# Kernel optimization log

Measured on AMD Instinct MI355X. Metric: run time of the kernel, lower is better.

Reference implementation:

```python
import jax, jax.numpy as jnp
import numpy as np

NN_SIZE = 16
RADIUS2 = 0.5 * 0.5  # radius^2
EPS = 0.0001


def setup_inputs() -> dict:
    key = jax.random.key(0)
    points = jax.random.normal(key, (4, 8192, 3), dtype=jnp.float32)
    return {"points": points}


def reference(points):
    # points: (B, N, 3)
    B, N, C = points.shape
    # Brute-force KNN (pytorch3d ops.knn_points with K = nn_size + 1, self included)
    sq = jnp.sum(points * points, axis=-1)  # (B, N)
    d2_all = sq[:, :, None] + sq[:, None, :] - 2.0 * jnp.einsum('bnc,bmc->bnm', points, points)  # (B,N,N)
    _, idx = jax.lax.top_k(-d2_all, NN_SIZE + 1)  # smallest distances first, (B,N,K+1)
    knn_idx = idx[:, :, 1:]  # drop self, (B, N, K)
    # Gather neighbor coordinates; detached in the original (.detach())
    knn_points = jax.vmap(lambda p, i: p[i])(points, knn_idx)  # (B, N, K, 3)
    knn_points = jax.lax.stop_gradient(knn_points)
    # Recompute squared distances (as the module does)
    knn_v = knn_points - points[:, :, None, :]  # (B, N, K, 3)
    distance2 = jnp.sum(knn_v * knn_v, axis=-1)  # (B, N, K)
    loss = 1.0 / jnp.sqrt(distance2 + EPS)
    loss = jnp.where(distance2 < RADIUS2, loss, jnp.zeros_like(loss))
    # reduction == 'mean'
    return jnp.mean(loss)
```

## Files before the change

### kernel.cpp

```cpp
#include <hip/hip_runtime.h>

#define NPTS 8192
#define NBATCH 4
#define NTOT (NBATCH * NPTS)
#define NN 16
#define RAD2 0.25f
#define EPSF 1e-4f
#define BIGF 1e30f

#define GC 16
#define GP 18
#define CBS 6144
#define NCELL_TOT (NBATCH * CBS)

#define STHR 256
#define SWV 4
#define SNB (NTOT / SWV)
#define HCAP 384

#define LOG2C 5.0103f
#define NCLAMP 257

#define WS_COUNTS 0
#define WS_RANGES (WS_COUNTS + NCELL_TOT * 4)
#define WS_CURSOR (WS_RANGES + NCELL_TOT * 8)
#define WS_SORTED (WS_CURSOR + NCELL_TOT * 4)
#define WS_BSUMS  (WS_SORTED + (NTOT + 64) * 16)
#define WS_NEEDED (WS_BSUMS + SNB * 4)

__device__ __forceinline__ int cellc(float v) {
  return min(max((int)floorf((v + 4.0f) * 2.0f), 0), GC - 1);
}

__device__ __forceinline__ float prsqrt(float x) {
  float r = __builtin_amdgcn_rsqf(x);
  r = r * fmaf(-0.5f * x * r, r, 1.5f);
  return r;
}

#define CE(a, b) { const float lo_ = fminf(a, b); const float hi_ = fmaxf(a, b); a = lo_; b = hi_; }


__global__ __launch_bounds__(256)
void zero_kernel(int* __restrict__ counts) {
  const int i = blockIdx.x * 256 + threadIdx.x;
  if (i < NCELL_TOT) counts[i] = 0;
}

__global__ __launch_bounds__(256)
void hist_kernel(const float* __restrict__ pts, int* __restrict__ counts) {
  const int i = blockIdx.x * 256 + threadIdx.x;
  if (i >= NTOT) return;
  const int b = i >> 13;
  const float x = pts[i * 3 + 0], y = pts[i * 3 + 1], z = pts[i * 3 + 2];
  const int c = b * CBS + ((cellc(z) + 1) * GP + (cellc(y) + 1)) * GP + (cellc(x) + 1);
  atomicAdd(&counts[c], 1);
}

__global__ __launch_bounds__(1024)
void scan_kernel(const int* __restrict__ counts, int2* __restrict__ ranges,
                 int* __restrict__ cursor) {
  __shared__ int wsum[16];
  __shared__ int woff[16];
  __shared__ int stot;
  const int b = blockIdx.x;
  const int tid = threadIdx.x;
  const int wid = tid >> 6;
  const int lane = tid & 63;
  const int g0 = b * CBS;
  int running = b * NPTS;
  for (int chunk = 0; chunk < CBS; chunk += 1024) {
    const int idx = chunk + tid;
    const int v = counts[g0 + idx];
    int x = v;
    for (int off = 1; off < 64; off <<= 1) {
      const int t = __shfl_up(x, off, 64);
      if (lane >= off) x += t;
    }
    if (lane == 63) wsum[wid] = x;
    __syncthreads();
    if (wid == 0) {
      int s = (lane < 16) ? wsum[lane] : 0;
      for (int off = 1; off < 16; off <<= 1) {
        const int t = __shfl_up(s, off, 64);
        if (lane >= off) s += t;
      }
      if (lane < 16) woff[lane] = s - wsum[lane];
      if (lane == 15) stot = s;
    }
    __syncthreads();
    const int excl = running + woff[wid] + x - v;
    ranges[g0 + idx] = make_int2(excl, v);
    cursor[g0 + idx] = excl;
    running += stot;
    __syncthreads();
  }
}

__global__ __launch_bounds__(256)
void scatter_kernel(const float* __restrict__ pts, int* __restrict__ cursor,
                    float4* __restrict__ sorted) {
  const int i = blockIdx.x * 256 + threadIdx.x;
  if (i >= NTOT) return;
  const int b = i >> 13;
  const float x = pts[i * 3 + 0], y = pts[i * 3 + 1], z = pts[i * 3 + 2];
  const int c = b * CBS + ((cellc(z) + 1) * GP + (cellc(y) + 1)) * GP + (cellc(x) + 1);
  const int pos = atomicAdd(&cursor[c], 1);
  sorted[pos] = make_float4(x, y, z, fmaf(x, x, fmaf(y, y, z * z)));
}


template<int R>
__device__ __forceinline__ float tourney(const float* __restrict__ hq, int hn, int lane) {
  float v[R];
#pragma unroll
  for (int r = 0; r < R; ++r) {
    const int idx = lane + 64 * r;
    v[r] = (idx < hn) ? hq[idx] : BIGF;
  }
  if constexpr (R == 3) { CE(v[0], v[1]); CE(v[1], v[2]); CE(v[0], v[1]); }
  if constexpr (R == 6) {
    CE(v[0], v[1]); CE(v[2], v[3]); CE(v[4], v[5]);
    CE(v[1], v[2]); CE(v[3], v[4]);
    CE(v[0], v[1]); CE(v[2], v[3]); CE(v[4], v[5]);
    CE(v[1], v[2]); CE(v[3], v[4]);
    CE(v[0], v[1]); CE(v[2], v[3]); CE(v[4], v[5]);
    CE(v[1], v[2]); CE(v[3], v[4]);
  }
  float loss = 0.0f;
#pragma unroll
  for (int r = 0; r < NN; ++r) {
    float g = v[0];
    g = fminf(g, __shfl_xor(g, 1));
    g = fminf(g, __shfl_xor(g, 2));
    g = fminf(g, __shfl_xor(g, 4));
    g = fminf(g, __shfl_xor(g, 8));
    g = fminf(g, __shfl_xor(g, 16));
    g = fminf(g, __shfl_xor(g, 32));
    loss += prsqrt(g + EPSF);
    const unsigned long long own = __ballot(v[0] == g);
    const int first = (int)(__ffsll((unsigned long long)own) - 1);
    if (lane == first) {
#pragma unroll
      for (int r2 = 0; r2 < R - 1; ++r2) v[r2] = v[r2 + 1];
      v[R - 1] = BIGF;
    }
  }
  return loss;
}

__global__ __launch_bounds__(STHR)
void search_kernel(const float4* __restrict__ sorted, const int2* __restrict__ rngs,
                   float* __restrict__ bsums) {
  __shared__ float hbuf[SWV][HCAP];
  __shared__ float wloss[SWV];

  const int tid = threadIdx.x;
  const int wv = tid >> 6;
  const int lane = tid & 63;
  const int p = blockIdx.x * SWV + wv;
  const int bb = p >> 13;

  const float4 pt = sorted[p];
  const float m2x = -2.0f * pt.x, m2y = -2.0f * pt.y, m2z = -2.0f * pt.z;
  const float sp = pt.w;
  const int cx = cellc(pt.x), cy = cellc(pt.y), cz = cellc(pt.z);
  const int c0 = __builtin_amdgcn_readfirstlane(
      bb * CBS + ((cz + 1) * GP + (cy + 1)) * GP + (cx + 1));

  const int rowoff[9] = {
    (-1 * GP - 1) * GP, (-1 * GP + 0) * GP, (-1 * GP + 1) * GP,
    ( 0 * GP - 1) * GP, ( 0 * GP + 0) * GP, ( 0 * GP + 1) * GP,
    ( 1 * GP - 1) * GP, ( 1 * GP + 0) * GP, ( 1 * GP + 1) * GP };

  int rs[9], re[9];
  int ncand = 0;
#pragma unroll
  for (int m = 0; m < 9; ++m) {
    const int2 a = rngs[c0 + rowoff[m] - 1];
    const int2 e2 = rngs[c0 + rowoff[m] + 1];
    rs[m] = a.x;
    re[m] = e2.x + e2.y;
    ncand += re[m] - rs[m];
  }

  const bool clamped = (ncand <= NCLAMP);
  float r0sq = RAD2;
  if (!clamped) {
    r0sq = exp2f((LOG2C - log2f((float)ncand)) * (2.0f / 3.0f));
  }

  float* hq = hbuf[wv];
  int hcnt = 0;

#define SCAN_ROWS(RR) {                                                         \
    hcnt = 0;                                                                   \
    _Pragma("unroll")                                                           \
    for (int m = 0; m < 9; ++m) {                                               \
      const int s = rs[m], e = re[m];                                           \
      for (int j0 = s; j0 < e; j0 += 64) {                                      \
        const int j = j0 + lane;                                                \
        float d2 = BIGF;                                                        \
        if (j < e) {                                                            \
          const float4 q = sorted[j];                                           \
          d2 = fmaf(q.x, m2x, fmaf(q.y, m2y, fmaf(q.z, m2z, q.w + sp)));        \
        }                                                                       \
        bool hit = (d2 < (RR));                                                 \
        if (m == 4) hit = hit && (j != p);            \
        const unsigned long long bal = __ballot(hit);                           \
        const int pre = __builtin_amdgcn_mbcnt_hi(                              \
            (unsigned)(bal >> 32), __builtin_amdgcn_mbcnt_lo((unsigned)bal, 0));\
        const int pos = hcnt + pre;                                             \
        if (hit && pos < HCAP) hq[pos] = d2;                                    \
        hcnt += (int)__popcll(bal);                                             \
      }                                                                         \
    }                                                                           \
  }

  SCAN_ROWS(r0sq);
  int hn = min(hcnt, HCAP);
  if (hn < NN && !clamped) {
    SCAN_ROWS(RAD2);
    hn = min(hcnt, HCAP);
  }

  float loss;
  if (hn <= 64) {
    float v = (lane < hn) ? hq[lane] : BIGF;
#pragma unroll
    for (int k = 2; k <= 64; k <<= 1) {
#pragma unroll
      for (int j = k >> 1; j > 0; j >>= 1) {
        const float o = __shfl_xor(v, j, 64);
        const bool keepmin = (((lane & j) == 0) != ((lane & k) != 0));
        v = keepmin ? fminf(v, o) : fmaxf(v, o);
      }
    }
    float l = (lane < NN && v < RAD2) ? prsqrt(v + EPSF) : 0.0f;
    l += __shfl_xor(l, 1);
    l += __shfl_xor(l, 2);
    l += __shfl_xor(l, 4);
    l += __shfl_xor(l, 8);
    l += __shfl_xor(l, 16);
    l += __shfl_xor(l, 32);
    loss = l;
  } else if (hn <= 192) {
    loss = tourney<3>(hq, hn, lane);
  } else {
    loss = tourney<6>(hq, hn, lane);
  }

  if (lane == 0) wloss[wv] = loss;
  __syncthreads();
  if (tid == 0) {
    float s = 0.0f;
#pragma unroll
    for (int w = 0; w < SWV; ++w) s += wloss[w];
    bsums[blockIdx.x] = s;
  }
}

__global__ __launch_bounds__(256)
void finalize_kernel(const float* __restrict__ block_sums, int nblocks,
                     float* __restrict__ out) {
  __shared__ float s[256];
  float v = 0.0f;
  for (int idx = threadIdx.x; idx < nblocks; idx += 256) v += block_sums[idx];
  s[threadIdx.x] = v;
  __syncthreads();
  for (int off = 128; off > 0; off >>= 1) {
    if (threadIdx.x < off) s[threadIdx.x] += s[threadIdx.x + off];
    __syncthreads();
  }
  if (threadIdx.x == 0) out[0] = s[0] / (float)(NBATCH * NPTS * NN);
}


#define DTILE 1024
#define DNT 512
#define DNW 8
#define DNB (NTOT / 64)
#define CSTRIDE 17
#define QTRIG 13

__device__ __forceinline__ void insert16(float (&td)[NN], float& thrmax, float v) {
  if (v < thrmax) {
    bool done = false;
#pragma unroll
    for (int k = 0; k < NN; ++k) {
      const bool hit = (!done) && (td[k] == thrmax);
      if (hit) td[k] = v;
      done = done || hit;
    }
    thrmax = td[0];
#pragma unroll
    for (int k = 1; k < NN; ++k) thrmax = fmaxf(thrmax, td[k]);
  }
}

__device__ __forceinline__ void drain_queue(float* buf, int qbase, int& cnt,
                                            float (&td)[NN], float& thrmax) {
#pragma unroll
  for (int c = 0; c < 16; ++c) {
    const float v = (c < cnt) ? buf[qbase + c] : BIGF;
    insert16(td, thrmax, v);
  }
  cnt = 0;
}

__global__ __launch_bounds__(DNT)
void dense_kernel(const float* __restrict__ pts, float* __restrict__ block_sums) {
  __shared__ float4 tile[DTILE];
  __shared__ float buf[DNT * CSTRIDE];

  const int tid = threadIdx.x;
  const int wave = tid >> 6;
  const int lane = tid & 63;
  const int bid = blockIdx.x;
  const int b = bid / (NPTS / 64);
  const int base = (bid % (NPTS / 64)) * 64;
  const float* __restrict__ bp = pts + (size_t)b * NPTS * 3;

  const int i = base + lane;
  const float xi = bp[i * 3 + 0];
  const float yi = bp[i * 3 + 1];
  const float zi = bp[i * 3 + 2];

  float td[NN];
#pragma unroll
  for (int k = 0; k < NN; ++k) td[k] = BIGF;
  float thrmax = BIGF;
  int cnt = 0;
  const int qbase = tid * CSTRIDE;

  for (int tb = 0; tb < NPTS; tb += DTILE) {
    for (int pp = tid; pp < DTILE; pp += DNT) {
      const float* sp = bp + (size_t)(tb + pp) * 3;
      tile[pp] = make_float4(sp[0], sp[1], sp[2], 0.0f);
    }
    __syncthreads();
    const int jb = wave * (DTILE / DNW);
    for (int jj = 0; jj < DTILE / DNW; ++jj) {
      const float4 q = tile[jb + jj];
      const float ddx = q.x - xi, ddy = q.y - yi, ddz = q.z - zi;
      const float d2 = fmaf(ddx, ddx, fmaf(ddy, ddy, ddz * ddz));
      if (d2 < RAD2 && d2 != 0.0f) {
        buf[qbase + cnt] = d2;
        ++cnt;
      }
      if (__any(cnt >= QTRIG)) drain_queue(buf, qbase, cnt, td, thrmax);
    }
    __syncthreads();
  }
  drain_queue(buf, qbase, cnt, td, thrmax);
#pragma unroll
  for (int k = 0; k < NN; ++k) buf[qbase + k] = td[k];
  __syncthreads();

  if (wave == 0) {
    float sd[NN];
#pragma unroll
    for (int k = 0; k < NN; ++k) sd[k] = BIGF;
    float smax = BIGF;
    for (int w = 0; w < DNW; ++w) {
      for (int c = 0; c < NN; ++c) {
        insert16(sd, smax, buf[(w * 64 + lane) * CSTRIDE + c]);
      }
    }
    float loss = 0.0f;
#pragma unroll
    for (int k = 0; k < NN; ++k) {
      if (sd[k] < RAD2) loss += 1.0f / sqrtf(sd[k] + EPSF);
    }
    for (int off = 32; off > 0; off >>= 1) loss += __shfl_down(loss, off);
    if (lane == 0) block_sums[bid] = loss;
  }
}


extern "C" void kernel_launch(void* const* d_in, const int* in_sizes, int n_in,
                              void* d_out, int out_size, void* d_ws, size_t ws_size,
                              hipStream_t stream) {
  const float* pts = (const float*)d_in[0];
  float* out = (float*)d_out;
  char* ws = (char*)d_ws;

  if (ws_size >= (size_t)WS_NEEDED) {
    int* counts = (int*)(ws + WS_COUNTS);
    int2* rngs = (int2*)(ws + WS_RANGES);
    int* cursor = (int*)(ws + WS_CURSOR);
    float4* sorted = (float4*)(ws + WS_SORTED);
    float* bsums = (float*)(ws + WS_BSUMS);

    zero_kernel<<<(NCELL_TOT + 255) / 256, 256, 0, stream>>>(counts);
    hist_kernel<<<(NTOT + 255) / 256, 256, 0, stream>>>(pts, counts);
    scan_kernel<<<NBATCH, 1024, 0, stream>>>(counts, rngs, cursor);
    scatter_kernel<<<(NTOT + 255) / 256, 256, 0, stream>>>(pts, cursor, sorted);
    search_kernel<<<SNB, STHR, 0, stream>>>(sorted, rngs, bsums);
    finalize_kernel<<<1, 256, 0, stream>>>(bsums, SNB, out);
  } else {
    float* bsums = (float*)ws;
    dense_kernel<<<DNB, DNT, 0, stream>>>(pts, bsums);
    finalize_kernel<<<1, 256, 0, stream>>>(bsums, DNB, out);
  }
}
```

Measured before the change: 66.87 us.

## Process two sorted query points per wavefront sharing candidate loads

Each wavefront now handles two consecutive sorted points. When both fall in the same y/z cell row, the union of their 3x3 x-ranges is scanned once, and each candidate load is used to compute distances for both queries. Otherwise the two points are scanned separately. This aims to halve candidate memory traffic and per-wave setup, at the cost of a wider scan range in the merged case and more registers and LDS per wave. The clamp radius in the merged case is derived from the combined candidate count, which may give different radius choices than per-point counts would.

```diff
diff --git a/kernel.cpp b/kernel.cpp
--- a/kernel.cpp
+++ b/kernel.cpp
@@ -15,7 +15,8 @@
 
 #define STHR 256
 #define SWV 4
-#define SNB (NTOT / SWV)
+#define PPW 2
+#define SNB (NTOT / (SWV * PPW))
 #define HCAP 384
 
 #define LOG2C 5.0103f
@@ -36,6 +37,11 @@
   float r = __builtin_amdgcn_rsqf(x);
   r = r * fmaf(-0.5f * x * r, r, 1.5f);
   return r;
+}
+
+__device__ __forceinline__ int lanepre(unsigned long long m) {
+  return __builtin_amdgcn_mbcnt_hi((unsigned)(m >> 32),
+         __builtin_amdgcn_mbcnt_lo((unsigned)m, 0));
 }
 
 #define CE(a, b) { const float lo_ = fminf(a, b); const float hi_ = fmaxf(a, b); a = lo_; b = hi_; }
@@ -110,6 +116,69 @@
 }
 
 
+__device__ __forceinline__ int scan1(const float4* __restrict__ sorted,
+    const int* rs, const int* re, float rr, int selfp,
+    float m2x, float m2y, float m2z, float sp, float* __restrict__ hq, int lane) {
+  int hcnt = 0;
+#pragma unroll
+  for (int m = 0; m < 9; ++m) {
+    const int s = rs[m], e = re[m];
+    for (int j0 = s; j0 < e; j0 += 64) {
+      const int j = j0 + lane;
+      float d2 = BIGF;
+      if (j < e) {
+        const float4 q = sorted[j];
+        d2 = fmaf(q.x, m2x, fmaf(q.y, m2y, fmaf(q.z, m2z, q.w + sp)));
+      }
+      const bool hit = (d2 < rr) && (j != selfp);
+      const unsigned long long bal = __ballot(hit);
+      const int pos = hcnt + lanepre(bal & ((1ull << lane) - 1ull) ? bal & ((1ull << lane) - 1ull) : 0ull);
+      const int pre = __popcll(bal & ((1ull << lane) - 1ull));
+      const int p2 = hcnt + pre;
+      if (hit && p2 < HCAP) hq[p2] = d2;
+      hcnt += (int)__popcll(bal);
+      (void)pos;
+    }
+  }
+  return hcnt;
+}
+
+__device__ __forceinline__ void scan2(const float4* __restrict__ sorted,
+    const int* rs, const int* re, float rr,
+    int pA, float m2xA, float m2yA, float m2zA, float spA,
+    int pB, float m2xB, float m2yB, float m2zB, float spB,
+    float* __restrict__ hqA, float* __restrict__ hqB, int lane,
+    int& hcntA, int& hcntB) {
+  int hA = 0, hB = 0;
+#pragma unroll
+  for (int m = 0; m < 9; ++m) {
+    const int s = rs[m], e = re[m];
+    for (int j0 = s; j0 < e; j0 += 64) {
+      const int j = j0 + lane;
+      float d2A = BIGF, d2B = BIGF;
+      if (j < e) {
+        const float4 q = sorted[j];
+        const float qw = q.w;
+        d2A = fmaf(q.x, m2xA, fmaf(q.y, m2yA, fmaf(q.z, m2zA, qw + spA)));
+        d2B = fmaf(q.x, m2xB, fmaf(q.y, m2yB, fmaf(q.z, m2zB, qw + spB)));
+      }
+      const unsigned long long below = (1ull << lane) - 1ull;
+      const bool hitA = (d2A < rr) && (j != pA);
+      const unsigned long long balA = __ballot(hitA);
+      const int posA = hA + (int)__popcll(balA & below);
+      if (hitA && posA < HCAP) hqA[posA] = d2A;
+      hA += (int)__popcll(balA);
+      const bool hitB = (d2B < rr) && (j != pB);
+      const unsigned long long balB = __ballot(hitB);
+      const int posB = hB + (int)__popcll(balB & below);
+      if (hitB && posB < HCAP) hqB[posB] = d2B;
+      hB += (int)__popcll(balB);
+    }
+  }
+  hcntA = hA;
+  hcntB = hB;
+}
+
 template<int R>
 __device__ __forceinline__ float tourney(const float* __restrict__ hq, int hn, int lane) {
   float v[R];
@@ -149,82 +218,7 @@
   return loss;
 }
 
-__global__ __launch_bounds__(STHR)
-void search_kernel(const float4* __restrict__ sorted, const int2* __restrict__ rngs,
-                   float* __restrict__ bsums) {
-  __shared__ float hbuf[SWV][HCAP];
-  __shared__ float wloss[SWV];
-
-  const int tid = threadIdx.x;
-  const int wv = tid >> 6;
-  const int lane = tid & 63;
-  const int p = blockIdx.x * SWV + wv;
-  const int bb = p >> 13;
-
-  const float4 pt = sorted[p];
-  const float m2x = -2.0f * pt.x, m2y = -2.0f * pt.y, m2z = -2.0f * pt.z;
-  const float sp = pt.w;
-  const int cx = cellc(pt.x), cy = cellc(pt.y), cz = cellc(pt.z);
-  const int c0 = __builtin_amdgcn_readfirstlane(
-      bb * CBS + ((cz + 1) * GP + (cy + 1)) * GP + (cx + 1));
-
-  const int rowoff[9] = {
-    (-1 * GP - 1) * GP, (-1 * GP + 0) * GP, (-1 * GP + 1) * GP,
-    ( 0 * GP - 1) * GP, ( 0 * GP + 0) * GP, ( 0 * GP + 1) * GP,
-    ( 1 * GP - 1) * GP, ( 1 * GP + 0) * GP, ( 1 * GP + 1) * GP };
-
-  int rs[9], re[9];
-  int ncand = 0;
-#pragma unroll
-  for (int m = 0; m < 9; ++m) {
-    const int2 a = rngs[c0 + rowoff[m] - 1];
-    const int2 e2 = rngs[c0 + rowoff[m] + 1];
-    rs[m] = a.x;
-    re[m] = e2.x + e2.y;
-    ncand += re[m] - rs[m];
-  }
-
-  const bool clamped = (ncand <= NCLAMP);
-  float r0sq = RAD2;
-  if (!clamped) {
-    r0sq = exp2f((LOG2C - log2f((float)ncand)) * (2.0f / 3.0f));
-  }
-
-  float* hq = hbuf[wv];
-  int hcnt = 0;
-
-#define SCAN_ROWS(RR) {                                                         \
-    hcnt = 0;                                                                   \
-    _Pragma("unroll")                                                           \
-    for (int m = 0; m < 9; ++m) {                                               \
-      const int s = rs[m], e = re[m];                                           \
-      for (int j0 = s; j0 < e; j0 += 64) {                                      \
-        const int j = j0 + lane;                                                \
-        float d2 = BIGF;                                                        \
-        if (j < e) {                                                            \
-          const float4 q = sorted[j];                                           \
-          d2 = fmaf(q.x, m2x, fmaf(q.y, m2y, fmaf(q.z, m2z, q.w + sp)));        \
-        }                                                                       \
-        bool hit = (d2 < (RR));                                                 \
-        if (m == 4) hit = hit && (j != p);            \
-        const unsigned long long bal = __ballot(hit);                           \
-        const int pre = __builtin_amdgcn_mbcnt_hi(                              \
-            (unsigned)(bal >> 32), __builtin_amdgcn_mbcnt_lo((unsigned)bal, 0));\
-        const int pos = hcnt + pre;                                             \
-        if (hit && pos < HCAP) hq[pos] = d2;                                    \
-        hcnt += (int)__popcll(bal);                                             \
-      }                                                                         \
-    }                                                                           \
-  }
-
-  SCAN_ROWS(r0sq);
-  int hn = min(hcnt, HCAP);
-  if (hn < NN && !clamped) {
-    SCAN_ROWS(RAD2);
-    hn = min(hcnt, HCAP);
-  }
-
-  float loss;
+__device__ __forceinline__ float extract_loss(const float* __restrict__ hq, int hn, int lane) {
   if (hn <= 64) {
     float v = (lane < hn) ? hq[lane] : BIGF;
 #pragma unroll
@@ -243,14 +237,106 @@
     l += __shfl_xor(l, 8);
     l += __shfl_xor(l, 16);
     l += __shfl_xor(l, 32);
-    loss = l;
+    return l;
   } else if (hn <= 192) {
-    loss = tourney<3>(hq, hn, lane);
+    return tourney<3>(hq, hn, lane);
+  }
+  return tourney<6>(hq, hn, lane);
+}
+
+
+__global__ __launch_bounds__(STHR)
+void search_kernel(const float4* __restrict__ sorted, const int2* __restrict__ rngs,
+                   float* __restrict__ bsums) {
+  __shared__ float hbuf[SWV][2][HCAP];
+  __shared__ float wloss[SWV];
+
+  const int tid = threadIdx.x;
+  const int wv = tid >> 6;
+  const int lane = tid & 63;
+  const int p0 = (blockIdx.x * SWV + wv) * 2;
+  const int p1 = p0 + 1;
+  const int bb = p0 >> 13;
+
+  const float4 ptA = sorted[p0];
+  const float4 ptB = sorted[p1];
+  const float m2xA = -2.0f * ptA.x, m2yA = -2.0f * ptA.y, m2zA = -2.0f * ptA.z;
+  const float spA = ptA.w;
+  const float m2xB = -2.0f * ptB.x, m2yB = -2.0f * ptB.y, m2zB = -2.0f * ptB.z;
+  const float spB = ptB.w;
+
+  const int rbA = __builtin_amdgcn_readfirstlane(
+      bb * CBS + ((cellc(ptA.z) + 1) * GP + (cellc(ptA.y) + 1)) * GP);
+  const int rbB = __builtin_amdgcn_readfirstlane(
+      bb * CBS + ((cellc(ptB.z) + 1) * GP + (cellc(ptB.y) + 1)) * GP);
+  const int xA = __builtin_amdgcn_readfirstlane(cellc(ptA.x));
+  const int xB = __builtin_amdgcn_readfirstlane(cellc(ptB.x));
+
+  const int rowoff[9] = {
+    (-1 * GP - 1) * GP, (-1 * GP + 0) * GP, (-1 * GP + 1) * GP,
+    ( 0 * GP - 1) * GP, ( 0 * GP + 0) * GP, ( 0 * GP + 1) * GP,
+    ( 1 * GP - 1) * GP, ( 1 * GP + 0) * GP, ( 1 * GP + 1) * GP };
+
+  float* hqA = hbuf[wv][0];
+  float* hqB = hbuf[wv][1];
+  int hnA, hnB;
+
+  if (rbA == rbB) {
+    const int lo = min(xA, xB);
+    const int hi = max(xA, xB) + 2;
+    int rs[9], re[9], ncand = 0;
+#pragma unroll
+    for (int m = 0; m < 9; ++m) {
+      const int base = rbA + rowoff[m];
+      const int2 a = rngs[base + lo];
+      const int2 b = rngs[base + hi];
+      rs[m] = a.x;
+      re[m] = b.x + b.y;
+      ncand += re[m] - rs[m];
+    }
+    const bool clamped = (ncand <= NCLAMP);
+    float r0sq = RAD2;
+    if (!clamped) r0sq = exp2f((LOG2C - log2f((float)ncand)) * (2.0f / 3.0f));
+
+    int hA, hB;
+    scan2(sorted, rs, re, r0sq, p0, m2xA, m2yA, m2zA, spA,
+          p1, m2xB, m2yB, m2zB, spB, hqA, hqB, lane, hA, hB);
+    hnA = min(hA, HCAP);
+    hnB = min(hB, HCAP);
+    if (hnA < NN && !clamped)
+      hnA = min(scan1(sorted, rs, re, RAD2, p0, m2xA, m2yA, m2zA, spA, hqA, lane), HCAP);
+    if (hnB < NN && !clamped)
+      hnB = min(scan1(sorted, rs, re, RAD2, p1, m2xB, m2yB, m2zB, spB, hqB, lane), HCAP);
   } else {
-    loss = tourney<6>(hq, hn, lane);
-  }
-
-  if (lane == 0) wloss[wv] = loss;
+    int rsA[9], reA[9], ncA = 0, rsB[9], reB[9], ncB = 0;
+#pragma unroll
+    for (int m = 0; m < 9; ++m) {
+      const int baseA = rbA + rowoff[m];
+      const int2 a0 = rngs[baseA + xA];
+      const int2 a1 = rngs[baseA + xA + 2];
+      rsA[m] = a0.x; reA[m] = a1.x + a1.y; ncA += reA[m] - rsA[m];
+      const int baseB = rbB + rowoff[m];
+      const int2 b0 = rngs[baseB + xB];
+      const int2 b1 = rngs[baseB + xB + 2];
+      rsB[m] = b0.x; reB[m] = b1.x + b1.y; ncB += reB[m] - rsB[m];
+    }
+    const bool clA = (ncA <= NCLAMP);
+    const bool clB = (ncB <= NCLAMP);
+    float rA = RAD2, rB = RAD2;
+    if (!clA) rA = exp2f((LOG2C - log2f((float)ncA)) * (2.0f / 3.0f));
+    if (!clB) rB = exp2f((LOG2C - log2f((float)ncB)) * (2.0f / 3.0f));
+    hnA = min(scan1(sorted, rsA, reA, rA, p0, m2xA, m2yA, m2zA, spA, hqA, lane), HCAP);
+    if (hnA < NN && !clA)
+      hnA = min(scan1(sorted, rsA, reA, RAD2, p0, m2xA, m2yA, m2zA, spA, hqA, lane), HCAP);
+    hnB = min(scan1(sorted, rsB, reB, rB, p1, m2xB, m2yB, m2zB, spB, hqB, lane), HCAP);
+    if (hnB < NN && !clB)
+      hnB = min(scan1(sorted, rsB, reB, RAD2, p1, m2xB, m2yB, m2zB, spB, hqB, lane), HCAP);
+  }
+
+  const float lossA = extract_loss(hqA, hnA, lane);
+  const float lossB = extract_loss(hqB, hnB, lane);
+
+  if (lane == 0) wloss[wv] = lossA + lossB;
   __syncthreads();
   if (tid == 0) {
     float s = 0.0f;
```

Measured after the change: 65.26 us. 1.02x faster.
